# Optimization experiments

Measured on AMD Instinct MI355X. Metric: run time of the kernel, lower is better.

## Reference

```python
import jax, jax.numpy as jnp
import numpy as np

N, T, H, E = 16384, 4, 64, 262144
NEG_SLOPE = 0.2  # LeakyReLU slope for GAT-style attention
LN_EPS = 1e-5


def setup_inputs() -> dict:
    key = jax.random.key(0)
    ks = jax.random.split(key, 24)
    p = {}
    p["pred"] = jax.random.normal(ks[0], (N, T, H), jnp.float32)
    p["ei_structural"] = jax.random.randint(ks[1], (2, E), 0, N, jnp.int32)
    p["ei_functional"] = jax.random.randint(ks[2], (2, E), 0, N, jnp.int32)
    scale = 1.0 / np.sqrt(H)
    i = 3
    for l in range(2):
        for et in ("s", "f"):
            p[f"W{l}{et}"] = (jax.random.normal(ks[i], (H, H), jnp.float32) * scale); i += 1
            p[f"a{l}{et}"] = (jax.random.normal(ks[i], (H,), jnp.float32) * scale); i += 1
        p[f"g{l}"] = jnp.ones((H,), jnp.float32)
        p[f"b{l}"] = jnp.zeros((H,), jnp.float32)
    return p


def _conv(x, ei, W, a, n_dst):
    """Attention-based ST graph conv, temporal_kernel_size=1 (per-step)."""
    h = jnp.einsum('nth,hd->ntd', x, W)          # [N,T,H] linear transform
    src, dst = ei[0], ei[1]
    he = h[src]                                   # [E,T,H] gather per edge
    logits = jax.nn.leaky_relu(jnp.einsum('eth,h->et', he, a), NEG_SLOPE)
    m = jax.ops.segment_max(logits, dst, num_segments=n_dst)     # [N,T]
    ex = jnp.exp(logits - m[dst])                 # stable softmax over incoming edges
    den = jax.ops.segment_sum(ex, dst, num_segments=n_dst)
    alpha = ex / den[dst]                         # [E,T]
    return jax.ops.segment_sum(alpha[..., None] * he, dst, num_segments=n_dst)


def _ln(x, g, b):
    mu = x.mean(-1, keepdims=True)
    v = x.var(-1, keepdims=True)
    return (x - mu) * jax.lax.rsqrt(v + LN_EPS) * g + b


def reference(pred, ei_structural, ei_functional,
              W0s, a0s, W0f, a0f, g0, b0,
              W1s, a1s, W1f, a1f, g1, b1):
    x = pred
    layers = ((W0s, a0s, W0f, a0f, g0, b0), (W1s, a1s, W1f, a1f, g1, b1))
    for (Ws, av, Wf, af, g, b) in layers:
        ms = _conv(x, ei_structural, Ws, av, N)
        mf = _conv(x, ei_functional, Wf, af, N)
        # sum(messages)/len(messages), residual, LayerNorm over H (dropout=identity in eval)
        x = _ln(x + 0.5 * (ms + mf), g, b)
    return x
```

## Files before the change

### kernel.cpp

```cpp
#include <hip/hip_runtime.h>
#include <hip/hip_bf16.h>

#define NN 16384
#define TT 4
#define HH 64
#define NT (NN * TT)
#define CAP 128
#define NEG_SLOPE 0.2f
#define LN_EPS 1e-5f

typedef __attribute__((ext_vector_type(8))) short short8;
typedef __attribute__((ext_vector_type(4))) float f32x4;

__device__ __forceinline__ float bf2f(unsigned short u) {
    return __uint_as_float((unsigned)u << 16);
}
__device__ __forceinline__ unsigned short f2bf(float f) {
    unsigned u = __float_as_uint(f);
    return (unsigned short)((u + 0x7FFF + ((u >> 16) & 1)) >> 16);
}


__global__ void zero_kernel(int* __restrict__ a, int n) {
    int i = blockIdx.x * blockDim.x + threadIdx.x;
    if (i < n) a[i] = 0;
}

__global__ void scatter_bucket_kernel(const int* __restrict__ ei_s, const int* __restrict__ ei_f,
                                      int* __restrict__ cnt2, int* __restrict__ col2, int E) {
    int e = blockIdx.x * blockDim.x + threadIdx.x;
    if (e < E) {
        int d = ei_s[E + e];
        int pos = atomicAdd(&cnt2[d], 1);
        if (pos < CAP) col2[d * CAP + pos] = ei_s[e];
    } else {
        e -= E;
        if (e < E) {
            int d = ei_f[E + e];
            int pos = atomicAdd(&cnt2[NN + d], 1);
            if (pos < CAP) col2[(long)NN * CAP + d * CAP + pos] = ei_f[e];
        }
    }
}


__global__ __launch_bounds__(256) void transform2_kernel(
    const float4* __restrict__ x4,
    const float* __restrict__ Ws, const float* __restrict__ as_,
    const float* __restrict__ Wf, const float* __restrict__ af,
    unsigned short* __restrict__ h_s, float* __restrict__ sc_s,
    unsigned short* __restrict__ h_f, float* __restrict__ sc_f) {
    const int lane = threadIdx.x & 63;
    const int wv = threadIdx.x >> 6;
    const int m = lane & 15;
    const int quad = lane >> 4;

    short8 Bs[4][2], Bf[4][2];
#pragma unroll
    for (int c = 0; c < 4; c++) {
#pragma unroll
        for (int ks = 0; ks < 2; ks++) {
#pragma unroll
            for (int j = 0; j < 8; j++) {
                int k = ks * 32 + quad * 8 + j;
                int n = c * 16 + m;
                Bs[c][ks][j] = (short)f2bf(Ws[k * 64 + n]);
                Bf[c][ks][j] = (short)f2bf(Wf[k * 64 + n]);
            }
        }
    }
    float a_s[4], a_f[4];
#pragma unroll
    for (int c = 0; c < 4; c++) { a_s[c] = as_[c * 16 + m]; a_f[c] = af[c * 16 + m]; }

    const int rowbase = blockIdx.x * 128 + wv * 32;
#pragma unroll
    for (int rt = 0; rt < 2; rt++) {
        const int row0 = rowbase + rt * 16;
        const long xbase = (long)(row0 + m) * 16 + quad * 2;
        float4 xa = x4[xbase];
        float4 xb = x4[xbase + 1];
        float4 xc = x4[xbase + 8];
        float4 xd = x4[xbase + 9];
        short8 A0, A1;
        A0[0] = (short)f2bf(xa.x); A0[1] = (short)f2bf(xa.y);
        A0[2] = (short)f2bf(xa.z); A0[3] = (short)f2bf(xa.w);
        A0[4] = (short)f2bf(xb.x); A0[5] = (short)f2bf(xb.y);
        A0[6] = (short)f2bf(xb.z); A0[7] = (short)f2bf(xb.w);
        A1[0] = (short)f2bf(xc.x); A1[1] = (short)f2bf(xc.y);
        A1[2] = (short)f2bf(xc.z); A1[3] = (short)f2bf(xc.w);
        A1[4] = (short)f2bf(xd.x); A1[5] = (short)f2bf(xd.y);
        A1[6] = (short)f2bf(xd.z); A1[7] = (short)f2bf(xd.w);

        f32x4 accs[4], accf[4];
#pragma unroll
        for (int c = 0; c < 4; c++) {
            accs[c] = (f32x4){0.f, 0.f, 0.f, 0.f};
            accf[c] = (f32x4){0.f, 0.f, 0.f, 0.f};
        }
#pragma unroll
        for (int c = 0; c < 4; c++) {
            accs[c] = __builtin_amdgcn_mfma_f32_16x16x32_bf16(A0, Bs[c][0], accs[c], 0, 0, 0);
            accs[c] = __builtin_amdgcn_mfma_f32_16x16x32_bf16(A1, Bs[c][1], accs[c], 0, 0, 0);
            accf[c] = __builtin_amdgcn_mfma_f32_16x16x32_bf16(A0, Bf[c][0], accf[c], 0, 0, 0);
            accf[c] = __builtin_amdgcn_mfma_f32_16x16x32_bf16(A1, Bf[c][1], accf[c], 0, 0, 0);
        }
#pragma unroll
        for (int reg = 0; reg < 4; reg++) {
            const int row = row0 + quad * 4 + reg;
            float ps = 0.f, pf = 0.f;
#pragma unroll
            for (int c = 0; c < 4; c++) {
                h_s[(long)row * 64 + c * 16 + m] = f2bf(accs[c][reg]);
                h_f[(long)row * 64 + c * 16 + m] = f2bf(accf[c][reg]);
                ps = fmaf(accs[c][reg], a_s[c], ps);
                pf = fmaf(accf[c][reg], a_f[c], pf);
            }
#pragma unroll
            for (int off = 1; off < 16; off <<= 1) {
                ps += __shfl_xor(ps, off, 64);
                pf += __shfl_xor(pf, off, 64);
            }
            if (m == 0) {
                sc_s[row] = (ps > 0.f) ? ps : NEG_SLOPE * ps;
                sc_f[row] = (pf > 0.f) ? pf : NEG_SLOPE * pf;
            }
        }
    }
}


__device__ __forceinline__ void agg_partial(const ushort4* __restrict__ h4,
                                            const float* __restrict__ sc,
                                            const int* __restrict__ col,
                                            int j, int jend, int t, int lane,
                                            float& den, float& ax, float& ay,
                                            float& az, float& aw) {
    for (; j + 8 <= jend; j += 8) {
        int s[8];
        float l[8];
        ushort4 hh[8];
#pragma unroll
        for (int u = 0; u < 8; u++) s[u] = col[j + u];
#pragma unroll
        for (int u = 0; u < 8; u++) l[u] = sc[s[u] * 4 + t];
#pragma unroll
        for (int u = 0; u < 8; u++) hh[u] = h4[s[u] * 64 + lane];
#pragma unroll
        for (int u = 0; u < 8; u++) {
            float e = __expf(l[u]);
            den += e;
            ax = fmaf(e, bf2f(hh[u].x), ax);
            ay = fmaf(e, bf2f(hh[u].y), ay);
            az = fmaf(e, bf2f(hh[u].z), az);
            aw = fmaf(e, bf2f(hh[u].w), aw);
        }
    }
    for (; j + 4 <= jend; j += 4) {
        int s[4];
        float l[4];
        ushort4 hh[4];
#pragma unroll
        for (int u = 0; u < 4; u++) s[u] = col[j + u];
#pragma unroll
        for (int u = 0; u < 4; u++) l[u] = sc[s[u] * 4 + t];
#pragma unroll
        for (int u = 0; u < 4; u++) hh[u] = h4[s[u] * 64 + lane];
#pragma unroll
        for (int u = 0; u < 4; u++) {
            float e = __expf(l[u]);
            den += e;
            ax = fmaf(e, bf2f(hh[u].x), ax);
            ay = fmaf(e, bf2f(hh[u].y), ay);
            az = fmaf(e, bf2f(hh[u].z), az);
            aw = fmaf(e, bf2f(hh[u].w), aw);
        }
    }
    for (; j < jend; j++) {
        int s0 = col[j];
        float l0 = sc[s0 * 4 + t];
        ushort4 h0 = h4[s0 * 64 + lane];
        float e0 = __expf(l0);
        den += e0;
        ax = fmaf(e0, bf2f(h0.x), ax);
        ay = fmaf(e0, bf2f(h0.y), ay);
        az = fmaf(e0, bf2f(h0.z), az);
        aw = fmaf(e0, bf2f(h0.w), aw);
    }
}

__global__ __launch_bounds__(256) void aggregate_kernel(
    const float4* __restrict__ x4,
    const ushort4* __restrict__ hs4, const float* __restrict__ scs,
    const int* __restrict__ cnts, const int* __restrict__ cols,
    const ushort4* __restrict__ hf4, const float* __restrict__ scf,
    const int* __restrict__ cntf, const int* __restrict__ colf,
    const float4* __restrict__ g4, const float4* __restrict__ b4,
    float4* __restrict__ out4) {
    __shared__ float4 accL[4][64];
    __shared__ float denL[4][64];
    const int wv = threadIdx.x >> 6;
    const int lane = threadIdx.x & 63;
    const int set = wv & 1;
    const int half = wv >> 1;
    const int n = blockIdx.x;
    const int t = lane >> 4;
    const int ci = lane & 15;

    const int* cnt = set ? cntf : cnts;
    const int* col = (set ? colf : cols) + (long)n * CAP;
    const ushort4* h4 = set ? hf4 : hs4;
    const float* sc = set ? scf : scs;

    int c = cnt[n];
    if (c > CAP) c = CAP;
    const int l0 = (c + 1) >> 1;
    const int j0 = half ? l0 : 0;
    const int j1 = half ? c : l0;

    float den = 0.f, ax = 0.f, ay = 0.f, az = 0.f, aw = 0.f;
    agg_partial(h4, sc, col, j0, j1, t, lane, den, ax, ay, az, aw);

    accL[wv][lane] = (float4){ax, ay, az, aw};
    denL[wv][lane] = den;
    __syncthreads();
    if (wv != 0) return;

    float4 a2 = accL[2][lane];
    float d_s = den + denL[2][lane];
    float4 a1 = accL[1][lane];
    float4 a3 = accL[3][lane];
    float d_f = denL[1][lane] + denL[3][lane];

    float msx = 0.f, msy = 0.f, msz = 0.f, msw = 0.f;
    if (d_s > 0.f) {
        float r = 1.f / d_s;
        msx = (ax + a2.x) * r; msy = (ay + a2.y) * r;
        msz = (az + a2.z) * r; msw = (aw + a2.w) * r;
    }
    float mfx = 0.f, mfy = 0.f, mfz = 0.f, mfw = 0.f;
    if (d_f > 0.f) {
        float r = 1.f / d_f;
        mfx = (a1.x + a3.x) * r; mfy = (a1.y + a3.y) * r;
        mfz = (a1.z + a3.z) * r; mfw = (a1.w + a3.w) * r;
    }

    float4 xv = x4[(long)n * 64 + lane];
    float v0 = xv.x + 0.5f * (msx + mfx);
    float v1 = xv.y + 0.5f * (msy + mfy);
    float v2 = xv.z + 0.5f * (msz + mfz);
    float v3 = xv.w + 0.5f * (msw + mfw);

    float sum = (v0 + v1) + (v2 + v3);
#pragma unroll
    for (int off = 1; off < 16; off <<= 1) sum += __shfl_xor(sum, off, 64);
    float mu = sum * (1.f / 64.f);
    float d0 = v0 - mu, d1 = v1 - mu, d2 = v2 - mu, d3 = v3 - mu;
    float var = (d0 * d0 + d1 * d1) + (d2 * d2 + d3 * d3);
#pragma unroll
    for (int off = 1; off < 16; off <<= 1) var += __shfl_xor(var, off, 64);
    var *= (1.f / 64.f);
    float inv = rsqrtf(var + LN_EPS);
    float4 gv = g4[ci], bv = b4[ci];
    float4 o;
    o.x = d0 * inv * gv.x + bv.x;
    o.y = d1 * inv * gv.y + bv.y;
    o.z = d2 * inv * gv.z + bv.z;
    o.w = d3 * inv * gv.w + bv.w;
    out4[(long)n * 64 + lane] = o;
}


extern "C" void kernel_launch(void* const* d_in, const int* in_sizes, int n_in,
                              void* d_out, int out_size, void* d_ws, size_t ws_size,
                              hipStream_t stream) {
    const float* pred = (const float*)d_in[0];
    const int* ei_s = (const int*)d_in[1];
    const int* ei_f = (const int*)d_in[2];
    const float* W0s = (const float*)d_in[3];
    const float* a0s = (const float*)d_in[4];
    const float* W0f = (const float*)d_in[5];
    const float* a0f = (const float*)d_in[6];
    const float* g0  = (const float*)d_in[7];
    const float* b0  = (const float*)d_in[8];
    const float* W1s = (const float*)d_in[9];
    const float* a1s = (const float*)d_in[10];
    const float* W1f = (const float*)d_in[11];
    const float* a1f = (const float*)d_in[12];
    const float* g1  = (const float*)d_in[13];
    const float* b1  = (const float*)d_in[14];
    const int E = in_sizes[1] / 2;

    char* ws = (char*)d_ws;
    auto alloc = [&](size_t bytes) {
        char* p = ws;
        ws += (bytes + 255) & ~(size_t)255;
        return p;
    };
    int* cnt2 = (int*)alloc((size_t)2 * NN * sizeof(int));
    int* col2 = (int*)alloc((size_t)2 * NN * CAP * sizeof(int));
    unsigned short* h_s = (unsigned short*)alloc((size_t)NT * HH * sizeof(unsigned short));
    unsigned short* h_f = (unsigned short*)alloc((size_t)NT * HH * sizeof(unsigned short));
    float* sc_s = (float*)alloc((size_t)NT * sizeof(float));
    float* sc_f = (float*)alloc((size_t)NT * sizeof(float));
    float* x_mid = (float*)alloc((size_t)NT * HH * sizeof(float));

    const int* cnt_s = cnt2;
    const int* cnt_f = cnt2 + NN;
    const int* col_s = col2;
    const int* col_f = col2 + (size_t)NN * CAP;

    const int EB = (E + 255) / 256;

    zero_kernel<<<(2 * NN) / 256, 256, 0, stream>>>(cnt2, 2 * NN);
    scatter_bucket_kernel<<<2 * EB, 256, 0, stream>>>(ei_s, ei_f, cnt2, col2, E);

    transform2_kernel<<<NT / 128, 256, 0, stream>>>(
        (const float4*)pred, W0s, a0s, W0f, a0f, h_s, sc_s, h_f, sc_f);
    aggregate_kernel<<<NN, 256, 0, stream>>>(
        (const float4*)pred, (const ushort4*)h_s, sc_s, cnt_s, col_s,
        (const ushort4*)h_f, sc_f, cnt_f, col_f,
        (const float4*)g0, (const float4*)b0, (float4*)x_mid);

    transform2_kernel<<<NT / 128, 256, 0, stream>>>(
        (const float4*)x_mid, W1s, a1s, W1f, a1f, h_s, sc_s, h_f, sc_f);
    aggregate_kernel<<<NN, 256, 0, stream>>>(
        (const float4*)x_mid, (const ushort4*)h_s, sc_s, cnt_s, col_s,
        (const ushort4*)h_f, sc_f, cnt_f, col_f,
        (const float4*)g1, (const float4*)b1, (float4*)d_out);
}
```

Baseline: 228.3 us.

## Precompute exp scores in transform; one wave per node handling both edge sets

The transform kernel now stores exp(leaky_relu(score)) per source row, so the aggregation no longer evaluates exp once per edge. The aggregate kernel is restructured so that each wave handles one whole node, interleaving structural and functional edges in blocks of four. This removes the shared-memory reduction and __syncthreads across four waves, and launches a quarter as many blocks. In exchange each wave does a longer serial loop, per-node load imbalance can grow, and skipping the max subtraction risks overflow for large logits.

```diff
diff --git a/kernel.cpp b/kernel.cpp
--- a/kernel.cpp
+++ b/kernel.cpp
@@ -48,8 +48,8 @@
     const float4* __restrict__ x4,
     const float* __restrict__ Ws, const float* __restrict__ as_,
     const float* __restrict__ Wf, const float* __restrict__ af,
-    unsigned short* __restrict__ h_s, float* __restrict__ sc_s,
-    unsigned short* __restrict__ h_f, float* __restrict__ sc_f) {
+    unsigned short* __restrict__ h_s, float* __restrict__ esc_s,
+    unsigned short* __restrict__ h_f, float* __restrict__ esc_f) {
     const int lane = threadIdx.x & 63;
     const int wv = threadIdx.x >> 6;
     const int m = lane & 15;
@@ -122,127 +122,101 @@
                 pf += __shfl_xor(pf, off, 64);
             }
             if (m == 0) {
-                sc_s[row] = (ps > 0.f) ? ps : NEG_SLOPE * ps;
-                sc_f[row] = (pf > 0.f) ? pf : NEG_SLOPE * pf;
-            }
-        }
-    }
-}
-
-
-__device__ __forceinline__ void agg_partial(const ushort4* __restrict__ h4,
-                                            const float* __restrict__ sc,
-                                            const int* __restrict__ col,
-                                            int j, int jend, int t, int lane,
-                                            float& den, float& ax, float& ay,
-                                            float& az, float& aw) {
-    for (; j + 8 <= jend; j += 8) {
-        int s[8];
-        float l[8];
-        ushort4 hh[8];
-#pragma unroll
-        for (int u = 0; u < 8; u++) s[u] = col[j + u];
-#pragma unroll
-        for (int u = 0; u < 8; u++) l[u] = sc[s[u] * 4 + t];
-#pragma unroll
-        for (int u = 0; u < 8; u++) hh[u] = h4[s[u] * 64 + lane];
-#pragma unroll
-        for (int u = 0; u < 8; u++) {
-            float e = __expf(l[u]);
-            den += e;
-            ax = fmaf(e, bf2f(hh[u].x), ax);
-            ay = fmaf(e, bf2f(hh[u].y), ay);
-            az = fmaf(e, bf2f(hh[u].z), az);
-            aw = fmaf(e, bf2f(hh[u].w), aw);
-        }
-    }
-    for (; j + 4 <= jend; j += 4) {
-        int s[4];
-        float l[4];
-        ushort4 hh[4];
-#pragma unroll
-        for (int u = 0; u < 4; u++) s[u] = col[j + u];
-#pragma unroll
-        for (int u = 0; u < 4; u++) l[u] = sc[s[u] * 4 + t];
-#pragma unroll
-        for (int u = 0; u < 4; u++) hh[u] = h4[s[u] * 64 + lane];
-#pragma unroll
-        for (int u = 0; u < 4; u++) {
-            float e = __expf(l[u]);
-            den += e;
-            ax = fmaf(e, bf2f(hh[u].x), ax);
-            ay = fmaf(e, bf2f(hh[u].y), ay);
-            az = fmaf(e, bf2f(hh[u].z), az);
-            aw = fmaf(e, bf2f(hh[u].w), aw);
-        }
-    }
-    for (; j < jend; j++) {
-        int s0 = col[j];
-        float l0 = sc[s0 * 4 + t];
-        ushort4 h0 = h4[s0 * 64 + lane];
-        float e0 = __expf(l0);
-        den += e0;
-        ax = fmaf(e0, bf2f(h0.x), ax);
-        ay = fmaf(e0, bf2f(h0.y), ay);
-        az = fmaf(e0, bf2f(h0.z), az);
-        aw = fmaf(e0, bf2f(h0.w), aw);
-    }
-}
+                float ls = (ps > 0.f) ? ps : NEG_SLOPE * ps;
+                float lf = (pf > 0.f) ? pf : NEG_SLOPE * pf;
+                esc_s[row] = __expf(ls);
+                esc_f[row] = __expf(lf);
+            }
+        }
+    }
+}
+
 
 __global__ __launch_bounds__(256) void aggregate_kernel(
     const float4* __restrict__ x4,
-    const ushort4* __restrict__ hs4, const float* __restrict__ scs,
+    const ushort4* __restrict__ hs4, const float* __restrict__ escs,
     const int* __restrict__ cnts, const int* __restrict__ cols,
-    const ushort4* __restrict__ hf4, const float* __restrict__ scf,
+    const ushort4* __restrict__ hf4, const float* __restrict__ escf,
     const int* __restrict__ cntf, const int* __restrict__ colf,
     const float4* __restrict__ g4, const float4* __restrict__ b4,
     float4* __restrict__ out4) {
-    __shared__ float4 accL[4][64];
-    __shared__ float denL[4][64];
     const int wv = threadIdx.x >> 6;
     const int lane = threadIdx.x & 63;
-    const int set = wv & 1;
-    const int half = wv >> 1;
-    const int n = blockIdx.x;
+    const int n = blockIdx.x * 4 + wv;
     const int t = lane >> 4;
     const int ci = lane & 15;
 
-    const int* cnt = set ? cntf : cnts;
-    const int* col = (set ? colf : cols) + (long)n * CAP;
-    const ushort4* h4 = set ? hf4 : hs4;
-    const float* sc = set ? scf : scs;
-
-    int c = cnt[n];
-    if (c > CAP) c = CAP;
-    const int l0 = (c + 1) >> 1;
-    const int j0 = half ? l0 : 0;
-    const int j1 = half ? c : l0;
-
-    float den = 0.f, ax = 0.f, ay = 0.f, az = 0.f, aw = 0.f;
-    agg_partial(h4, sc, col, j0, j1, t, lane, den, ax, ay, az, aw);
-
-    accL[wv][lane] = (float4){ax, ay, az, aw};
-    denL[wv][lane] = den;
-    __syncthreads();
-    if (wv != 0) return;
-
-    float4 a2 = accL[2][lane];
-    float d_s = den + denL[2][lane];
-    float4 a1 = accL[1][lane];
-    float4 a3 = accL[3][lane];
-    float d_f = denL[1][lane] + denL[3][lane];
+    int cS = cnts[n]; if (cS > CAP) cS = CAP;
+    int cF = cntf[n]; if (cF > CAP) cF = CAP;
+    const int* colS = cols + (long)n * CAP;
+    const int* colF = colf + (long)n * CAP;
+
+    float dS = 0.f, sx = 0.f, sy = 0.f, sz = 0.f, sw = 0.f;
+    float dF = 0.f, fx = 0.f, fy = 0.f, fz = 0.f, fw = 0.f;
+
+    const int nbS = (cS + 3) >> 2;
+    const int nbF = (cF + 3) >> 2;
+    const int nb = nbS > nbF ? nbS : nbF;
+
+    for (int it = 0; it < nb; ++it) {
+        const int j = it << 2;
+        const bool doS = it < nbS;
+        const bool doF = it < nbF;
+        int sS[4], sF[4];
+        float eS[4], eF[4];
+        ushort4 hS[4], hF[4];
+
+        if (doS) {
+#pragma unroll
+            for (int u = 0; u < 4; u++) { int idx = j + u; sS[u] = colS[idx < cS ? idx : cS - 1]; }
+        }
+        if (doF) {
+#pragma unroll
+            for (int u = 0; u < 4; u++) { int idx = j + u; sF[u] = colF[idx < cF ? idx : cF - 1]; }
+        }
+        if (doS) {
+#pragma unroll
+            for (int u = 0; u < 4; u++) { float e = escs[sS[u] * 4 + t]; eS[u] = (j + u < cS) ? e : 0.f; }
+#pragma unroll
+            for (int u = 0; u < 4; u++) hS[u] = hs4[(long)sS[u] * 64 + lane];
+        }
+        if (doF) {
+#pragma unroll
+            for (int u = 0; u < 4; u++) { float e = escf[sF[u] * 4 + t]; eF[u] = (j + u < cF) ? e : 0.f; }
+#pragma unroll
+            for (int u = 0; u < 4; u++) hF[u] = hf4[(long)sF[u] * 64 + lane];
+        }
+        if (doS) {
+#pragma unroll
+            for (int u = 0; u < 4; u++) {
+                dS += eS[u];
+                sx = fmaf(eS[u], bf2f(hS[u].x), sx);
+                sy = fmaf(eS[u], bf2f(hS[u].y), sy);
+                sz = fmaf(eS[u], bf2f(hS[u].z), sz);
+                sw = fmaf(eS[u], bf2f(hS[u].w), sw);
+            }
+        }
+        if (doF) {
+#pragma unroll
+            for (int u = 0; u < 4; u++) {
+                dF += eF[u];
+                fx = fmaf(eF[u], bf2f(hF[u].x), fx);
+                fy = fmaf(eF[u], bf2f(hF[u].y), fy);
+                fz = fmaf(eF[u], bf2f(hF[u].z), fz);
+                fw = fmaf(eF[u], bf2f(hF[u].w), fw);
+            }
+        }
+    }
 
     float msx = 0.f, msy = 0.f, msz = 0.f, msw = 0.f;
-    if (d_s > 0.f) {
-        float r = 1.f / d_s;
-        msx = (ax + a2.x) * r; msy = (ay + a2.y) * r;
-        msz = (az + a2.z) * r; msw = (aw + a2.w) * r;
+    if (dS > 0.f) {
+        float r = 1.f / dS;
+        msx = sx * r; msy = sy * r; msz = sz * r; msw = sw * r;
     }
     float mfx = 0.f, mfy = 0.f, mfz = 0.f, mfw = 0.f;
-    if (d_f > 0.f) {
-        float r = 1.f / d_f;
-        mfx = (a1.x + a3.x) * r; mfy = (a1.y + a3.y) * r;
-        mfz = (a1.z + a3.z) * r; mfw = (a1.w + a3.w) * r;
+    if (dF > 0.f) {
+        float r = 1.f / dF;
+        mfx = fx * r; mfy = fy * r; mfz = fz * r; mfw = fw * r;
     }
 
     float4 xv = x4[(long)n * 64 + lane];
@@ -301,8 +275,8 @@
     int* col2 = (int*)alloc((size_t)2 * NN * CAP * sizeof(int));
     unsigned short* h_s = (unsigned short*)alloc((size_t)NT * HH * sizeof(unsigned short));
     unsigned short* h_f = (unsigned short*)alloc((size_t)NT * HH * sizeof(unsigned short));
-    float* sc_s = (float*)alloc((size_t)NT * sizeof(float));
-    float* sc_f = (float*)alloc((size_t)NT * sizeof(float));
+    float* esc_s = (float*)alloc((size_t)NT * sizeof(float));
+    float* esc_f = (float*)alloc((size_t)NT * sizeof(float));
     float* x_mid = (float*)alloc((size_t)NT * HH * sizeof(float));
 
     const int* cnt_s = cnt2;
@@ -316,16 +290,16 @@
     scatter_bucket_kernel<<<2 * EB, 256, 0, stream>>>(ei_s, ei_f, cnt2, col2, E);
 
     transform2_kernel<<<NT / 128, 256, 0, stream>>>(
-        (const float4*)pred, W0s, a0s, W0f, a0f, h_s, sc_s, h_f, sc_f);
-    aggregate_kernel<<<NN, 256, 0, stream>>>(
-        (const float4*)pred, (const ushort4*)h_s, sc_s, cnt_s, col_s,
-        (const ushort4*)h_f, sc_f, cnt_f, col_f,
+        (const float4*)pred, W0s, a0s, W0f, a0f, h_s, esc_s, h_f, esc_f);
+    aggregate_kernel<<<NN / 4, 256, 0, stream>>>(
+        (const float4*)pred, (const ushort4*)h_s, esc_s, cnt_s, col_s,
+        (const ushort4*)h_f, esc_f, cnt_f, col_f,
         (const float4*)g0, (const float4*)b0, (float4*)x_mid);
 
     transform2_kernel<<<NT / 128, 256, 0, stream>>>(
-        (const float4*)x_mid, W1s, a1s, W1f, a1f, h_s, sc_s, h_f, sc_f);
-    aggregate_kernel<<<NN, 256, 0, stream>>>(
-        (const float4*)x_mid, (const ushort4*)h_s, sc_s, cnt_s, col_s,
-        (const ushort4*)h_f, sc_f, cnt_f, col_f,
+        (const float4*)x_mid, W1s, a1s, W1f, a1f, h_s, esc_s, h_f, esc_f);
+    aggregate_kernel<<<NN / 4, 256, 0, stream>>>(
+        (const float4*)x_mid, (const ushort4*)h_s, esc_s, cnt_s, col_s,
+        (const ushort4*)h_f, esc_f, cnt_f, col_f,
         (const float4*)g1, (const float4*)b1, (float4*)d_out);
 }
```

Result: no change. 227.5 us (-0.3%).
